# Kernel tuning notes

Measured on AMD Instinct MI355X. Metric: run time of the kernel, lower is better.

The kernel has to match this reference:

```python
import jax, jax.numpy as jnp
import numpy as np

B, N, DIM, H, DH, K = 4, 2048, 512, 6, 64, 16
KEEP_PROB = 0.9  # 1 - dropout_rate
LOG2PI = float(np.log(2.0 * np.pi))
LOG_PRIOR = float(np.log(1.0 / K))


def setup_inputs() -> dict:
    key = jax.random.key(0)
    ks = jax.random.split(key, 7)
    inputs_q = jax.random.normal(ks[0], (B, N, DIM), dtype=jnp.float32)
    # decoder-style causal mask, shape [B, 1, q_len, kv_len]
    causal = jnp.tril(jnp.ones((N, N), dtype=jnp.float32))
    mask = jnp.broadcast_to(causal[None, None], (B, 1, N, N))
    # dropout keep mask broadcast across the query dim: [B, H, 1, kv_len]
    keep = jax.random.bernoulli(ks[1], KEEP_PROB, (B, H, 1, N)).astype(jnp.float32)
    w_qkv = jax.random.normal(ks[2], (DIM, 3 * H * DH), dtype=jnp.float32) * 0.02
    w_out = jax.random.normal(ks[3], (H * DH, DIM), dtype=jnp.float32) * 0.02
    mu_lookup = jax.random.normal(ks[4], (K, DIM), dtype=jnp.float32)
    logvar_lookup = jax.random.normal(ks[5], (K, DIM), dtype=jnp.float32) * 0.1
    return {
        "inputs_q": inputs_q,
        "mask": mask,
        "keep": keep,
        "w_qkv": w_qkv,
        "w_out": w_out,
        "mu_lookup": mu_lookup,
        "logvar_lookup": logvar_lookup,
    }


def reference(inputs_q, mask, keep, w_qkv, w_out, mu_lookup, logvar_lookup):
    # --- MultiHeadDotProductAttention (self-attn path) ---
    qkv = (inputs_q @ w_qkv).reshape(B, N, 3, H, DH)  # [B,N,3,H,DH]
    q, k, v = qkv[:, :, 0], qkv[:, :, 1], qkv[:, :, 2]
    # bias: 0 where mask > 0, -1e10 elsewhere (note: no 1/sqrt(d) scaling, as in source)
    bias = jnp.where(mask > 0, 0.0, -1e10)
    attn_weights = jnp.einsum('bqhd,bkhd->bhqk', q, k) + bias  # [B,H,N,N]
    attn_weights = jax.nn.softmax(attn_weights, axis=-1)
    # broadcast dropout: mask shared across the query dim
    attn_weights = attn_weights * keep / KEEP_PROB
    attn_out = jnp.einsum('bhqk,bkhd->bqhd', attn_weights, v)
    attn_out = attn_out.reshape(B, N, H * DH) @ w_out  # [B,N,DIM]

    # --- GMM posterior approx q(y|x) ~= p(y|z) (approx_qy_x, vectorized over k) ---
    z = attn_out.mean(axis=1)  # pooled latent, [B,DIM]
    diff = z[:, None, :] - mu_lookup[None]  # [B,K,DIM]
    llh = -0.5 * jnp.sum(
        diff * diff / jnp.exp(logvar_lookup)[None] + logvar_lookup[None] + LOG2PI,
        axis=-1,
    )  # [B,K]
    logLogit_qy_x = llh + LOG_PRIOR
    qy_x = jax.nn.softmax(logLogit_qy_x, axis=1)  # [B,K]

    # combine mixture mean back in so both branches are live in one output
    return attn_out + (qy_x @ mu_lookup)[:, None, :]
```

## Files before the change

### kernel.cpp

```cpp
#include <hip/hip_runtime.h>
#include <cstdint>
#include <cstddef>

#define NH 6
#define NSEQ 2048
#define DIMD 512
#define BATCH 4
#define HD 384
#define LOG2PI_F 1.8378770664093453f
#define LOG2E_F 1.4426950408889634f
#define M12L2_F (-17.312340490667562f)

typedef __attribute__((ext_vector_type(8))) short short8;
typedef __attribute__((ext_vector_type(8))) unsigned short ushort8;
typedef __attribute__((ext_vector_type(4))) unsigned short ushort4v;
typedef __attribute__((ext_vector_type(4))) float floatx4;
typedef __attribute__((ext_vector_type(2))) unsigned int uint2v;

__device__ inline unsigned short f2bf(float f){
  unsigned int u = __float_as_uint(f);
  u += 0x7FFFu + ((u>>16)&1u);
  return (unsigned short)(u>>16);
}

#define GLD16(gp, lp) __builtin_amdgcn_global_load_lds( \
  (const __attribute__((address_space(1))) void*)(gp), \
  (__attribute__((address_space(3))) void*)(lp), 16, 0, 0)

__device__ inline void wtrans_body(
    const float* __restrict__ src, unsigned short* __restrict__ dst,
    int R, int C, int bx, int by, unsigned short* Ls, int t)
{
  const int r = t>>2, c0 = (t&3)*16;
  const int d0 = by*64, n0 = bx*64;
  #pragma unroll
  for (int j=0;j<16;j+=4){
    floatx4 v = *(const floatx4*)(src + (size_t)(d0+r)*C + n0 + c0 + j);
    #pragma unroll
    for(int jj=0;jj<4;jj++) Ls[r*72 + c0+j+jj] = f2bf(v[jj]);
  }
  __syncthreads();
  #pragma unroll
  for (int j=0;j<16;j+=8){
    ushort8 o;
    #pragma unroll
    for(int jj=0;jj<8;jj++) o[jj] = Ls[(c0+j+jj)*72 + r];
    *(ushort8*)(dst + (size_t)(n0+r)*R + d0 + c0 + j) = o;
  }
}

__global__ __launch_bounds__(256) void prep(
    const float* __restrict__ xq, unsigned short* __restrict__ xbf,
    const float* __restrict__ w_qkv, unsigned short* __restrict__ wqT,
    const float* __restrict__ w_out, unsigned short* __restrict__ woT)
{
  __shared__ __attribute__((aligned(16))) unsigned short Ls[64*72];
  const int bid = blockIdx.x, t = threadIdx.x;
  if (bid < 4096){
    int i = bid*256 + t;
    floatx4 v = *(const floatx4*)(xq + (size_t)i*4);
    ushort4v r;
    #pragma unroll
    for(int j=0;j<4;j++) r[j] = f2bf(v[j]);
    *(ushort4v*)(xbf + (size_t)i*4) = r;
  } else if (bid < 4240){
    int rb = bid - 4096;
    wtrans_body(w_qkv, wqT, 512, 1152, rb%18, rb/18, Ls, t);
  } else {
    int rb = bid - 4240;
    wtrans_body(w_out, woT, 384, 512, rb%8, rb/8, Ls, t);
  }
}

__global__ __launch_bounds__(256) void gemm_qkv(
    const unsigned short* __restrict__ A,
    const unsigned short* __restrict__ Bt,
    const float* __restrict__ keep,
    unsigned short* __restrict__ Qo, unsigned short* __restrict__ Ko,
    unsigned short* __restrict__ Vt)
{
  __shared__ __attribute__((aligned(16))) unsigned short Cs[128*132];
  unsigned short* As = Cs;
  unsigned short* Bs = Cs + 128*64;
  const int tid = threadIdx.x;
  const int w = tid>>6, lane = tid&63;
  const int wr = w>>1, wc = w&1;
  const int quad = lane>>4, l16 = lane&15;
  const int tM = blockIdx.x*128, tN = blockIdx.y*128;
  const int r8 = lane>>3, c8 = (lane&7)*8;
  floatx4 acc[4][4];
  floatx4 zed = {0.f,0.f,0.f,0.f};
  #pragma unroll
  for (int i=0;i<4;i++)
    #pragma unroll
    for(int j=0;j<4;j++) acc[i][j] = zed;

  for (int k0=0; k0<512; k0+=64){
    #pragma unroll
    for (int i=0;i<4;i++){
      int row = w*32 + i*8;
      GLD16(A  + (size_t)(tM+row+r8)*512 + k0 + c8, As + row*64);
      GLD16(Bt + (size_t)(tN+row+r8)*512 + k0 + c8, Bs + row*64);
    }
    __syncthreads();
    #pragma unroll
    for (int kk=0; kk<64; kk+=32){
      short8 af[4], bf[4];
      #pragma unroll
      for(int mt=0;mt<4;mt++)
        af[mt] = *(const short8*)(As + (wr*64+mt*16+l16)*64 + kk + quad*8);
      #pragma unroll
      for(int nt=0;nt<4;nt++)
        bf[nt] = *(const short8*)(Bs + (wc*64+nt*16+l16)*64 + kk + quad*8);
      #pragma unroll
      for(int mt=0;mt<4;mt++)
        #pragma unroll
        for(int nt=0;nt<4;nt++)
          acc[mt][nt] = __builtin_amdgcn_mfma_f32_16x16x32_bf16(af[mt], bf[nt], acc[mt][nt], 0,0,0);
    }
    __syncthreads();
  }
  #pragma unroll
  for(int mt=0;mt<4;mt++)
    #pragma unroll
    for(int nt=0;nt<4;nt++){
      int gcol = tN + wc*64 + nt*16 + l16;
      float qs = (gcol < 384) ? LOG2E_F : 1.0f;
      #pragma unroll
      for(int r=0;r<4;r++)
        Cs[(wr*64+mt*16+quad*4+r)*132 + wc*64+nt*16+l16] = f2bf(acc[mt][nt][r]*qs);
    }
  __syncthreads();
  if (blockIdx.y < 6){
    const int row = tid>>1, colh = (tid&1)*64;
    const int gcol0 = tN + colh;
    const int t = gcol0/384, rem = gcol0 - t*384, h = rem>>6;
    const int grow = tM + row, b = grow>>11, n = grow & 2047;
    unsigned short* dst = (t==0 ? Qo : Ko) + ((size_t)((b*NH+h)*NSEQ+n))*64;
    #pragma unroll
    for(int j=0;j<8;j++)
      *(ushort8*)(dst + j*8) = *(const ushort8*)(Cs + row*132 + colh + j*8);
  } else {
    const int dcol = tid>>1;
    const int nh   = (tid&1)*64;
    const int gcol = tN + dcol;
    const int rem = gcol - 768, h = rem>>6, dh = rem&63;
    const int b = tM>>11, nb = tM & 2047;
    const float* kp = keep + (size_t)(b*NH+h)*NSEQ + nb + nh;
    unsigned short* dst = Vt + ((size_t)((b*NH+h)*64 + dh))*NSEQ + nb + nh;
    #pragma unroll
    for (int j8=0;j8<8;j8++){
      floatx4 k0 = *(const floatx4*)(kp + j8*8);
      floatx4 k1 = *(const floatx4*)(kp + j8*8 + 4);
      ushort8 o;
      #pragma unroll
      for(int u=0;u<4;u++)
        o[u]   = (k0[u] < 0.5f) ? (unsigned short)0 : Cs[(nh + j8*8 + u)*132 + dcol];
      #pragma unroll
      for(int u=0;u<4;u++)
        o[4+u] = (k1[u] < 0.5f) ? (unsigned short)0 : Cs[(nh + j8*8 + 4 + u)*132 + dcol];
      *(ushort8*)(dst + j8*8) = o;
    }
  }
}

__global__ __launch_bounds__(256, 3) void attn_kernel(
    const unsigned short* __restrict__ Qg, const unsigned short* __restrict__ Kg,
    const unsigned short* __restrict__ VtG,
    unsigned short* __restrict__ atp)
{
  __shared__ __attribute__((aligned(16))) char sm[4*32*68*4 + 4*32*4];
  const int tid = threadIdx.x;
  const int w = tid>>6, lane = tid&63;
  unsigned short* Ps = (unsigned short*)sm + w*(32*72);
  float* Oc   = (float*)sm;
  float* accs = (float*)(sm + 4*32*68*4);
  const int quad = lane>>4, l16 = lane&15;
  const int bid = blockIdx.x;
  const int idx = bid>>3;
  const int bh  = (bid&7) + 8*(idx % 3);
  const int c   = 63 - idx/3;
  const int b = bh/NH, h = bh - b*NH;
  const unsigned short* Qb = Qg  + (size_t)bh*NSEQ*64;
  const int q0 = c*32;
  const int nkt = (c>>1) + 1;
  const int q_abs0 = q0 + l16;

  const unsigned short* Kl = Kg  + (size_t)bh*NSEQ*64 + (size_t)l16*64 + quad*8;
  const unsigned short* Vl = VtG + (size_t)bh*64*NSEQ + (size_t)l16*NSEQ + quad*8;
  unsigned short* Psw = Ps + l16*72 + quad*4;
  const unsigned short* Psr = Ps + l16*72 + quad*8;

  short8 qf[2][2];
  #pragma unroll
  for(int mt=0;mt<2;mt++)
    #pragma unroll
    for(int kc=0;kc<2;kc++)
      qf[mt][kc] = *(const short8*)(Qb + (size_t)(q0+mt*16+l16)*64 + kc*32 + quad*8);

  short8 onesf;
  #pragma unroll
  for(int j=0;j<8;j++) onesf[j] = (short)0x3F80;

  floatx4 O[2][4];
  floatx4 accl[2];
  floatx4 zed = {0.f,0.f,0.f,0.f};
  floatx4 m12v = {M12L2_F, M12L2_F, M12L2_F, M12L2_F};
  #pragma unroll
  for(int mt=0;mt<2;mt++){
    #pragma unroll
    for(int dt=0;dt<4;dt++) O[mt][dt] = zed;
    accl[mt] = zed;
  }

  for (int kt = w; kt < nkt; kt += 4){
    const int kB = kt*64;
    short8 vf[2][4];
    const unsigned short* vp0 = Vl + kB;
    #pragma unroll
    for(int kh=0;kh<2;kh++)
      #pragma unroll
      for(int dt=0;dt<4;dt++)
        vf[kh][dt] = *(const short8*)(vp0 + (size_t)dt*32768 + kh*32);

    floatx4 sacc[2][4];
    #pragma unroll
    for(int mt=0;mt<2;mt++)
      #pragma unroll
      for(int nt=0;nt<4;nt++) sacc[mt][nt] = m12v;
    const unsigned short* kp0 = Kl + (size_t)kt*4096;
    #pragma unroll
    for(int nt=0;nt<4;nt++){
      short8 kf0 = *(const short8*)(kp0 + nt*1024);
      short8 kf1 = *(const short8*)(kp0 + nt*1024 + 32);
      #pragma unroll
      for(int mt=0;mt<2;mt++){
        sacc[mt][nt] = __builtin_amdgcn_mfma_f32_16x16x32_bf16(kf0, qf[mt][0], sacc[mt][nt], 0,0,0);
        sacc[mt][nt] = __builtin_amdgcn_mfma_f32_16x16x32_bf16(kf1, qf[mt][1], sacc[mt][nt], 0,0,0);
      }
    }

    const bool dia = (kt == nkt-1);
    #pragma unroll
    for(int mt=0;mt<2;mt++){
      const int qa = q_abs0 + mt*16;
      #pragma unroll
      for(int nt=0;nt<4;nt++){
        const int key0 = kB + nt*16 + quad*4;
        float p0 = exp2f(sacc[mt][nt][0]);
        float p1 = exp2f(sacc[mt][nt][1]);
        float p2 = exp2f(sacc[mt][nt][2]);
        float p3 = exp2f(sacc[mt][nt][3]);
        if (dia){
          p0 = (key0   <= qa) ? p0 : 0.f;
          p1 = (key0+1 <= qa) ? p1 : 0.f;
          p2 = (key0+2 <= qa) ? p2 : 0.f;
          p3 = (key0+3 <= qa) ? p3 : 0.f;
        }
        unsigned int lo, hi;
        asm("v_cvt_pk_bf16_f32 %0, %1, %2" : "=v"(lo) : "v"(p0), "v"(p1));
        asm("v_cvt_pk_bf16_f32 %0, %1, %2" : "=v"(hi) : "v"(p2), "v"(p3));
        uint2v pk; pk[0] = lo; pk[1] = hi;
        *(uint2v*)(Psw + mt*1152 + nt*16) = pk;
      }
    }
    #pragma unroll
    for(int kh=0;kh<2;kh++){
      #pragma unroll
      for(int mt=0;mt<2;mt++){
        short8 pf = *(const short8*)(Psr + mt*1152 + kh*32);
        accl[mt] = __builtin_amdgcn_mfma_f32_16x16x32_bf16(pf, onesf, accl[mt], 0,0,0);
        #pragma unroll
        for(int dt=0;dt<4;dt++)
          O[mt][dt] = __builtin_amdgcn_mfma_f32_16x16x32_bf16(pf, vf[kh][dt], O[mt][dt], 0,0,0);
      }
    }
  }

  __syncthreads();
  {
    float* Ow = Oc + w*(32*68);
    #pragma unroll
    for(int mt=0;mt<2;mt++){
      #pragma unroll
      for(int dt=0;dt<4;dt++)
        #pragma unroll
        for(int r=0;r<4;r++)
          Ow[(mt*16+quad*4+r)*68 + dt*16 + l16] = O[mt][dt][r];
      if (l16 == 0){
        #pragma unroll
        for(int r=0;r<4;r++)
          accs[w*32 + mt*16+quad*4+r] = accl[mt][r];
      }
    }
  }
  __syncthreads();

  const int orow = tid>>3, oc0 = (tid&7)*8;
  float as = accs[0*32+orow] + accs[1*32+orow] + accs[2*32+orow] + accs[3*32+orow];
  float sc2 = (1.0f/0.9f) / as;
  float vsum[8];
  #pragma unroll
  for(int j=0;j<8;j++) vsum[j] = 0.f;
  #pragma unroll
  for(int s=0;s<4;s++){
    const float* p = Oc + s*(32*68) + orow*68 + oc0;
    #pragma unroll
    for(int j=0;j<8;j++) vsum[j] += p[j];
  }
  ushort8 o;
  #pragma unroll
  for(int j=0;j<8;j++) o[j] = f2bf(vsum[j]*sc2);
  unsigned short* dstp = atp + ((size_t)(b*NSEQ + q0 + orow))*HD + h*64 + oc0;
  *(ushort8*)dstp = o;
}

__global__ __launch_bounds__(256) void gemm_proj(
    const unsigned short* __restrict__ A,
    const unsigned short* __restrict__ Bt,
    float* __restrict__ out,
    float* __restrict__ z)
{
  __shared__ __attribute__((aligned(16))) unsigned short As[128*64];
  __shared__ __attribute__((aligned(16))) unsigned short Bs[128*64];
  const int tid = threadIdx.x;
  const int w = tid>>6, lane = tid&63;
  const int wr = w>>1, wc = w&1;
  const int quad = lane>>4, l16 = lane&15;
  const int tM = blockIdx.x*128, tN = blockIdx.y*128;
  const int r8 = lane>>3, c8 = (lane&7)*8;
  floatx4 acc[4][4];
  floatx4 zed = {0.f,0.f,0.f,0.f};
  #pragma unroll
  for (int i=0;i<4;i++)
    #pragma unroll
    for(int j=0;j<4;j++) acc[i][j] = zed;

  for (int k0=0; k0<384; k0+=64){
    #pragma unroll
    for (int i=0;i<4;i++){
      int row = w*32 + i*8;
      GLD16(A  + (size_t)(tM+row+r8)*384 + k0 + c8, As + row*64);
      GLD16(Bt + (size_t)(tN+row+r8)*384 + k0 + c8, Bs + row*64);
    }
    __syncthreads();
    #pragma unroll
    for (int kk=0; kk<64; kk+=32){
      short8 af[4], bf[4];
      #pragma unroll
      for(int mt=0;mt<4;mt++)
        af[mt] = *(const short8*)(As + (wr*64+mt*16+l16)*64 + kk + quad*8);
      #pragma unroll
      for(int nt=0;nt<4;nt++)
        bf[nt] = *(const short8*)(Bs + (wc*64+nt*16+l16)*64 + kk + quad*8);
      #pragma unroll
      for(int mt=0;mt<4;mt++)
        #pragma unroll
        for(int nt=0;nt<4;nt++)
          acc[mt][nt] = __builtin_amdgcn_mfma_f32_16x16x32_bf16(af[mt], bf[nt], acc[mt][nt], 0,0,0);
    }
    __syncthreads();
  }
  #pragma unroll
  for(int mt=0;mt<4;mt++){
    int grow = tM + wr*64 + mt*16 + quad*4;
    #pragma unroll
    for(int nt=0;nt<4;nt++){
      int gcol = tN + wc*64 + nt*16 + l16;
      #pragma unroll
      for(int r=0;r<4;r++)
        out[(size_t)(grow+r)*512 + gcol] = acc[mt][nt][r];
    }
  }
  #pragma unroll
  for(int nt=0;nt<4;nt++){
    float s = 0.f;
    #pragma unroll
    for(int mt=0;mt<4;mt++)
      #pragma unroll
      for(int r=0;r<4;r++) s += acc[mt][nt][r];
    s += __shfl_xor(s, 16, 64);
    s += __shfl_xor(s, 32, 64);
    if (quad == 0){
      int gcol = tN + wc*64 + nt*16 + l16;
      atomicAdd(&z[(tM>>11)*DIMD + gcol], s);
    }
  }
}

__global__ __launch_bounds__(256) void gmm_kernel(
    const float* __restrict__ z, const float* __restrict__ mu,
    const float* __restrict__ lv, float* __restrict__ c)
{
  __shared__ float sh[16];
  __shared__ float qy[16];
  int tid = threadIdx.x;
  int k = tid>>4, li = tid&15;
  int b = blockIdx.x;
  float part = 0.f;
  for(int d=li; d<DIMD; d+=16){
    float zz = z[b*DIMD+d] * (1.0f/2048.0f);
    float m = mu[k*DIMD+d], l = lv[k*DIMD+d];
    float diff = zz - m;
    part += diff*diff*__expf(-l) + l + LOG2PI_F;
  }
  #pragma unroll
  for(int off=8;off>=1;off>>=1) part += __shfl_xor(part, off, 64);
  if (li==0) sh[k] = part;
  __syncthreads();
  if (tid<16){
    float logit = -0.5f*sh[tid];
    float mx = logit;
    #pragma unroll
    for(int off=8;off>=1;off>>=1) mx = fmaxf(mx, __shfl_xor(mx, off, 64));
    float e = __expf(logit-mx);
    float se = e;
    #pragma unroll
    for(int off=8;off>=1;off>>=1) se += __shfl_xor(se, off, 64);
    qy[tid] = e/se;
  }
  __syncthreads();
  for(int d=tid; d<DIMD; d+=256){
    float accv = 0.f;
    #pragma unroll
    for(int kk=0;kk<16;kk++) accv += qy[kk]*mu[kk*DIMD+d];
    c[b*DIMD+d] = accv;
  }
}

__global__ __launch_bounds__(256) void final_add(
    float* __restrict__ out, const float* __restrict__ c)
{
  size_t i = ((size_t)blockIdx.x*256 + threadIdx.x)*4;
  int d = (int)(i & 511);
  int b = (int)(i >> 20);
  floatx4 a = *(const floatx4*)(out + i);
  floatx4 cc = *(const floatx4*)(c + b*DIMD + d);
  *(floatx4*)(out + i) = a + cc;
}

extern "C" void kernel_launch(void* const* d_in, const int* in_sizes, int n_in,
                              void* d_out, int out_size, void* d_ws, size_t ws_size,
                              hipStream_t stream) {
  const float* inputs_q = (const float*)d_in[0];
  const float* keep  = (const float*)d_in[2];
  const float* w_qkv = (const float*)d_in[3];
  const float* w_out = (const float*)d_in[4];
  const float* mu    = (const float*)d_in[5];
  const float* lv    = (const float*)d_in[6];
  float* out = (float*)d_out;
  char* ws = (char*)d_ws;
  size_t off = 0;
  auto alloc = [&](size_t bytes){ void* p = ws + off; off += (bytes + 255) & ~(size_t)255; return p; };
  unsigned short* Qb  = (unsigned short*)alloc((size_t)24*2048*64*2);
  unsigned short* Kb  = (unsigned short*)alloc((size_t)24*2048*64*2);
  unsigned short* Vt  = (unsigned short*)alloc((size_t)24*64*2048*2);
  unsigned short* xbf = (unsigned short*)alloc((size_t)8192*512*2);
  unsigned short* wqT = (unsigned short*)alloc((size_t)1152*512*2);
  unsigned short* woT = (unsigned short*)alloc((size_t)512*384*2);
  unsigned short* atp = (unsigned short*)alloc((size_t)8192*384*2);
  float* z  = (float*)alloc((size_t)4*512*4);
  float* c  = (float*)alloc((size_t)4*512*4);

  hipMemsetAsync(z, 0, 4*512*4, stream);
  prep<<<4288, 256, 0, stream>>>(inputs_q, xbf, w_qkv, wqT, w_out, woT);
  gemm_qkv<<<dim3(64,9), 256, 0, stream>>>(xbf, wqT, keep, Qb, Kb, Vt);
  attn_kernel<<<1536, 256, 0, stream>>>(Qb, Kb, Vt, atp);
  gemm_proj<<<dim3(64,4), 256, 0, stream>>>(atp, woT, out, z);
  gmm_kernel<<<4, 256, 0, stream>>>(z, mu, lv, c);
  final_add<<<4096, 256, 0, stream>>>(out, c);
}
```

Baseline: 234.7 us.

## Replace LDS P round-trip with permlane swaps and scalar row-sum reduction

The softmax probability tile no longer goes through shared memory. It is rearranged from the QK^T MFMA output layout into the PV MFMA operand layout in registers with v_permlane32_swap/v_permlane16_swap. The row-sum, previously computed by an extra MFMA against a ones vector, becomes a per-lane float accumulation finished with cross-lane shuffles. This removes LDS stores and loads, one MFMA per step, and the first __syncthreads. The row sum is now taken from fp32 values rather than bf16-rounded ones, so it can differ slightly from the bf16 P actually used in the PV product.

```diff
diff --git a/kernel.cpp b/kernel.cpp
--- a/kernel.cpp
+++ b/kernel.cpp
@@ -15,7 +15,6 @@
 typedef __attribute__((ext_vector_type(8))) unsigned short ushort8;
 typedef __attribute__((ext_vector_type(4))) unsigned short ushort4v;
 typedef __attribute__((ext_vector_type(4))) float floatx4;
-typedef __attribute__((ext_vector_type(2))) unsigned int uint2v;
 
 __device__ inline unsigned short f2bf(float f){
   unsigned int u = __float_as_uint(f);
@@ -172,7 +171,6 @@
   __shared__ __attribute__((aligned(16))) char sm[4*32*68*4 + 4*32*4];
   const int tid = threadIdx.x;
   const int w = tid>>6, lane = tid&63;
-  unsigned short* Ps = (unsigned short*)sm + w*(32*72);
   float* Oc   = (float*)sm;
   float* accs = (float*)(sm + 4*32*68*4);
   const int quad = lane>>4, l16 = lane&15;
@@ -188,8 +186,6 @@
 
   const unsigned short* Kl = Kg  + (size_t)bh*NSEQ*64 + (size_t)l16*64 + quad*8;
   const unsigned short* Vl = VtG + (size_t)bh*64*NSEQ + (size_t)l16*NSEQ + quad*8;
-  unsigned short* Psw = Ps + l16*72 + quad*4;
-  const unsigned short* Psr = Ps + l16*72 + quad*8;
 
   short8 qf[2][2];
   #pragma unroll
@@ -198,20 +194,14 @@
     for(int kc=0;kc<2;kc++)
       qf[mt][kc] = *(const short8*)(Qb + (size_t)(q0+mt*16+l16)*64 + kc*32 + quad*8);
 
-  short8 onesf;
-  #pragma unroll
-  for(int j=0;j<8;j++) onesf[j] = (short)0x3F80;
-
   floatx4 O[2][4];
-  floatx4 accl[2];
+  float accl[2] = {0.f, 0.f};
   floatx4 zed = {0.f,0.f,0.f,0.f};
   floatx4 m12v = {M12L2_F, M12L2_F, M12L2_F, M12L2_F};
   #pragma unroll
-  for(int mt=0;mt<2;mt++){
+  for(int mt=0;mt<2;mt++)
     #pragma unroll
     for(int dt=0;dt<4;dt++) O[mt][dt] = zed;
-    accl[mt] = zed;
-  }
 
   for (int kt = w; kt < nkt; kt += 4){
     const int kB = kt*64;
@@ -244,6 +234,8 @@
     #pragma unroll
     for(int mt=0;mt<2;mt++){
       const int qa = q_abs0 + mt*16;
+      unsigned int d0[4], d1[4];
+      float rs = 0.f;
       #pragma unroll
       for(int nt=0;nt<4;nt++){
         const int key0 = kB + nt*16 + quad*4;
@@ -257,19 +249,22 @@
           p2 = (key0+2 <= qa) ? p2 : 0.f;
           p3 = (key0+3 <= qa) ? p3 : 0.f;
         }
-        unsigned int lo, hi;
-        asm("v_cvt_pk_bf16_f32 %0, %1, %2" : "=v"(lo) : "v"(p0), "v"(p1));
-        asm("v_cvt_pk_bf16_f32 %0, %1, %2" : "=v"(hi) : "v"(p2), "v"(p3));
-        uint2v pk; pk[0] = lo; pk[1] = hi;
-        *(uint2v*)(Psw + mt*1152 + nt*16) = pk;
+        rs += (p0+p1) + (p2+p3);
+        asm("v_cvt_pk_bf16_f32 %0, %1, %2" : "=v"(d0[nt]) : "v"(p0), "v"(p1));
+        asm("v_cvt_pk_bf16_f32 %0, %1, %2" : "=v"(d1[nt]) : "v"(p2), "v"(p3));
       }
-    }
-    #pragma unroll
-    for(int kh=0;kh<2;kh++){
-      #pragma unroll
-      for(int mt=0;mt<2;mt++){
-        short8 pf = *(const short8*)(Psr + mt*1152 + kh*32);
-        accl[mt] = __builtin_amdgcn_mfma_f32_16x16x32_bf16(pf, onesf, accl[mt], 0,0,0);
+      accl[mt] += rs;
+      #pragma unroll
+      for(int kh=0;kh<2;kh++){
+        unsigned int x0 = d0[2*kh],   x1 = d1[2*kh];
+        unsigned int y0 = d0[2*kh+1], y1 = d1[2*kh+1];
+        asm("v_permlane32_swap_b32 %0, %1" : "+v"(x0), "+v"(y0));
+        asm("v_permlane16_swap_b32 %0, %1" : "+v"(x0), "+v"(y0));
+        asm("v_permlane32_swap_b32 %0, %1" : "+v"(x1), "+v"(y1));
+        asm("v_permlane16_swap_b32 %0, %1" : "+v"(x1), "+v"(y1));
+        union { unsigned int u[4]; short8 s; } cvt;
+        cvt.u[0] = x0; cvt.u[1] = x1; cvt.u[2] = y0; cvt.u[3] = y1;
+        short8 pf = cvt.s;
         #pragma unroll
         for(int dt=0;dt<4;dt++)
           O[mt][dt] = __builtin_amdgcn_mfma_f32_16x16x32_bf16(pf, vf[kh][dt], O[mt][dt], 0,0,0);
@@ -277,7 +272,12 @@
     }
   }
 
-  __syncthreads();
+  #pragma unroll
+  for(int mt=0;mt<2;mt++){
+    accl[mt] += __shfl_xor(accl[mt], 16, 64);
+    accl[mt] += __shfl_xor(accl[mt], 32, 64);
+  }
+
   {
     float* Ow = Oc + w*(32*68);
     #pragma unroll
@@ -287,11 +287,8 @@
         #pragma unroll
         for(int r=0;r<4;r++)
           Ow[(mt*16+quad*4+r)*68 + dt*16 + l16] = O[mt][dt][r];
-      if (l16 == 0){
-        #pragma unroll
-        for(int r=0;r<4;r++)
-          accs[w*32 + mt*16+quad*4+r] = accl[mt][r];
-      }
+      if (quad == 0)
+        accs[w*32 + mt*16 + l16] = accl[mt];
     }
   }
   __syncthreads();
```

Result: no change. 234.9 us (+0.1%).
